# Kernel optimization log

Hardware: AMD Instinct MI355X
Metric: run time of the kernel (lower is better)

Reference implementation:

```python
import jax, jax.numpy as jnp
import numpy as np

N_HEADS = 16  # must match init_kwargs
BIAS_SCALE = 0.1


def _src_grid(out_size, in_size):
    # torch F.interpolate bilinear, align_corners=False semantics
    scale = in_size / out_size
    src = jnp.clip((jnp.arange(out_size, dtype=jnp.float32) + 0.5) * scale - 0.5, 0.0)
    i0 = jnp.minimum(jnp.floor(src).astype(jnp.int32), in_size - 1)
    i1 = jnp.minimum(i0 + 1, in_size - 1)
    w = src - i0.astype(jnp.float32)
    return i0, i1, w


def _bilinear_resize(img, out_h, out_w):
    Hin, Win = img.shape[-2], img.shape[-1]
    r0, r1, wy = _src_grid(out_h, Hin)
    c0, c1, wx = _src_grid(out_w, Win)
    rows = img[:, r0, :] * (1.0 - wy)[None, :, None] + img[:, r1, :] * wy[None, :, None]
    return rows[:, :, c0] * (1.0 - wx)[None, None, :] + rows[:, :, c1] * wx[None, None, :]


def setup_inputs() -> dict:
    key = jax.random.key(0)
    ks = jax.random.split(key, 10)
    B, L, D, M, K = 4, 1024, 1024, 64, 32
    s = 0.02
    return {
        "x": jax.random.normal(ks[0], (B, L, D), dtype=jnp.float32),
        "harmonics": jax.random.normal(ks[1], (B, M, K), dtype=jnp.float32),
        "wq": jax.random.normal(ks[2], (D, D), dtype=jnp.float32) * s,
        "bq": jax.random.normal(ks[3], (D,), dtype=jnp.float32) * s,
        "wk": jax.random.normal(ks[4], (D, D), dtype=jnp.float32) * s,
        "bk": jax.random.normal(ks[5], (D,), dtype=jnp.float32) * s,
        "wv": jax.random.normal(ks[6], (D, D), dtype=jnp.float32) * s,
        "bv": jax.random.normal(ks[7], (D,), dtype=jnp.float32) * s,
        "wo": jax.random.normal(ks[8], (D, D), dtype=jnp.float32) * s,
        "bo": jax.random.normal(ks[9], (D,), dtype=jnp.float32) * s,
    }


def reference(x, harmonics, wq, bq, wk, bk, wv, bv, wo, bo):
    B, L, D = x.shape
    hd = D // N_HEADS
    scaling = hd ** -0.5

    def split_heads(t):  # [B, L, D] -> [B, H, L, hd]
        return t.reshape(B, L, N_HEADS, hd).transpose(0, 2, 1, 3)

    q = split_heads(x @ wq.T + bq)
    k = split_heads(x @ wk.T + bk)
    v = split_heads(x @ wv.T + bv)

    scores = jnp.einsum("bhqd,bhkd->bhqk", q, k) * scaling  # [B, H, L, L]

    gram = jnp.einsum("bmk,bnk->bmn", harmonics, harmonics)  # [B, M, M]
    bias = _bilinear_resize(gram, L, L)  # [B, L, L]
    scores = scores + BIAS_SCALE * bias[:, None, :, :]

    attn = jax.nn.softmax(scores, axis=-1)
    out = jnp.einsum("bhqk,bhkd->bhqd", attn, v)  # [B, H, L, hd]
    out = out.transpose(0, 2, 1, 3).reshape(B, L, D)
    return out @ wo.T + bo
```

## Files before the change

### kernel.cpp

```cpp
#include <hip/hip_runtime.h>


using short8  = __attribute__((ext_vector_type(8))) short;
using short4v = __attribute__((ext_vector_type(4))) short;
using float4v = __attribute__((ext_vector_type(4))) float;

#define MFMA16(a, b, c) __builtin_amdgcn_mfma_f32_16x16x32_bf16((a), (b), (c), 0, 0, 0)

#define LOG2E 1.44269504088896f

static __device__ __forceinline__ short f2bf(float f) {
    union { float f; unsigned u; } v; v.f = f;
    unsigned r = v.u + 0x7fffu + ((v.u >> 16) & 1u);
    return (short)(r >> 16);
}

static __device__ __forceinline__ unsigned pack2bf(float lo, float hi) {
    union { float f; unsigned u; } a, b;
    a.f = lo; b.f = hi;
    return __builtin_amdgcn_perm(b.u + 0x8000u, a.u + 0x8000u, 0x07060302u);
}

static __device__ __forceinline__ void dma16(const short* g, short* l) {
    __builtin_amdgcn_global_load_lds((const __attribute__((address_space(1))) void*)g,
                                     (__attribute__((address_space(3))) void*)l, 16, 0, 0);
}

__global__ __launch_bounds__(256) void convert_all(
    const float* __restrict__ x,  const float* __restrict__ wq,
    const float* __restrict__ wk, const float* __restrict__ wv,
    const float* __restrict__ wo, short* __restrict__ xb, short* __restrict__ wb) {
    int idx = blockIdx.x * 256 + threadIdx.x;
    for (int i = idx; i < 2097152; i += gridDim.x * 256) {
        const float* src; short* dst;
        if (i < 1048576) {
            src = x + (size_t)i * 4;
            dst = xb + (size_t)i * 4;
        } else {
            int j = i - 1048576;
            int sel = j >> 18;
            const float* w = (sel == 0) ? wq : (sel == 1) ? wk : (sel == 2) ? wv : wo;
            src = w + (size_t)(j & 262143) * 4;
            dst = wb + (size_t)j * 4;
        }
        float4v v = *(const float4v*)src;
        short4v o;
        o.x = f2bf(v.x); o.y = f2bf(v.y); o.z = f2bf(v.z); o.w = f2bf(v.w);
        *(short4v*)dst = o;
    }
}

__global__ __launch_bounds__(256) void fill_aug(const float* __restrict__ harm,
                                                short* __restrict__ Qp,
                                                short* __restrict__ Kp) {
    int b  = blockIdx.y;
    int lc = blockIdx.x;
    int tid = threadIdx.x;
    int ll = tid >> 3;
    int d8 = (tid & 7) * 8;
    int l  = lc * 32 + ll;

    __shared__ float hs[64][33];
    for (int i = tid; i < 2048; i += 256) hs[i >> 5][i & 31] = harm[(size_t)b * 2048 + i];
    __syncthreads();

    float src = (l + 0.5f) * 0.0625f - 0.5f;
    if (src < 0.f) src = 0.f;
    int r0 = (int)floorf(src); if (r0 > 63) r0 = 63;
    int r1 = r0 + 1;           if (r1 > 63) r1 = 63;
    float wy = src - (float)r0;

    float hr[32];
    #pragma unroll
    for (int k = 0; k < 32; k++) hr[k] = (1.f - wy) * hs[r0][k] + wy * hs[r1][k];

    short8 qa, ka;
    #pragma unroll
    for (int j = 0; j < 8; j++) {
        float g = 0.f;
        #pragma unroll
        for (int k = 0; k < 32; k++) g += hr[k] * hs[d8 + j][k];
        qa[j] = f2bf(0.1f * LOG2E * g);
    }
    #pragma unroll
    for (int j = 0; j < 8; j++) {
        float vv = 0.f;
        if (d8 + j == r0) vv += 1.f - wy;
        if (d8 + j == r1) vv += wy;
        ka[j] = f2bf(vv);
    }
    for (int h = 0; h < 16; h++) {
        size_t base = (((size_t)(b * 16 + h) * 1024 + l) << 7) + 64 + d8;
        *(short8*)(Qp + base) = qa;
        *(short8*)(Kp + base) = ka;
    }
}

template <int MODE>
__global__ __launch_bounds__(256, 2) void gemm_kernel(
    const short* __restrict__ A,
    const short* __restrict__ Wb,
    const float* __restrict__ B0, const float* __restrict__ B1, const float* __restrict__ B2,
    short* __restrict__ Qp, short* __restrict__ Kp, short* __restrict__ Vp,
    float* __restrict__ outF) {
    const int z = blockIdx.z;
    const short* W  = Wb + (size_t)z * 1048576;
    const float* Bs = (z == 0) ? B0 : ((z == 1) ? B1 : B2);

    __shared__ short Sm[2][8192];

    const int tid  = threadIdx.x;
    const int lane = tid & 63;
    const int wv   = tid >> 6;
    const int wm   = (wv >> 1) * 64;
    const int wn   = (wv & 1) * 64;
    const int l16  = lane & 15;
    const int quad = lane >> 4;
    const int bm   = blockIdx.x * 128;
    const int bn   = blockIdx.y * 128;

    const short* aSrc[2];
    const short* wSrc[2];
    #pragma unroll
    for (int j = 0; j < 2; j++) {
        int c = j * 256 + tid;
        int r = c >> 2, gs = (c & 3) ^ ((r >> 1) & 3);
        aSrc[j] = A + (size_t)(bm + r) * 1024 + gs * 8;
        wSrc[j] = W + (size_t)(bn + r) * 1024 + gs * 8;
    }
    const int fr = (quad ^ ((l16 >> 1) & 3)) * 8;
    int ai[4], bi[4];
    #pragma unroll
    for (int t = 0; t < 4; t++) {
        ai[t] = (wm + t * 16 + l16) * 32 + fr;
        bi[t] = 4096 + (wn + t * 16 + l16) * 32 + fr;
    }

    float4v zero4 = {0.f, 0.f, 0.f, 0.f};
    float4v acc[4][4];
    #pragma unroll
    for (int i = 0; i < 4; i++)
        #pragma unroll
        for (int j = 0; j < 4; j++) acc[i][j] = zero4;

    dma16(aSrc[0], &Sm[0][wv * 512]);
    dma16(aSrc[1], &Sm[0][2048 + wv * 512]);
    dma16(wSrc[0], &Sm[0][4096 + wv * 512]);
    dma16(wSrc[1], &Sm[0][6144 + wv * 512]);
    #pragma unroll
    for (int j = 0; j < 2; j++) { aSrc[j] += 32; wSrc[j] += 32; }
    __syncthreads();

    for (int kt = 0; kt < 32; kt++) {
        const int cur = kt & 1, nxt = cur ^ 1;
        if (kt < 31) {
            dma16(aSrc[0], &Sm[nxt][wv * 512]);
            dma16(aSrc[1], &Sm[nxt][2048 + wv * 512]);
            dma16(wSrc[0], &Sm[nxt][4096 + wv * 512]);
            dma16(wSrc[1], &Sm[nxt][6144 + wv * 512]);
            #pragma unroll
            for (int j = 0; j < 2; j++) { aSrc[j] += 32; wSrc[j] += 32; }
        }

        short8 af[4], bfr[4];
        #pragma unroll
        for (int mt = 0; mt < 4; mt++) af[mt]  = *(const short8*)&Sm[cur][ai[mt]];
        #pragma unroll
        for (int nt = 0; nt < 4; nt++) bfr[nt] = *(const short8*)&Sm[cur][bi[nt]];
        #pragma unroll
        for (int mt = 0; mt < 4; mt++)
            #pragma unroll
            for (int nt = 0; nt < 4; nt++)
                acc[mt][nt] = MFMA16(af[mt], bfr[nt], acc[mt][nt]);

        __syncthreads();
    }

    #pragma unroll
    for (int mt = 0; mt < 4; mt++)
        #pragma unroll
        for (int nt = 0; nt < 4; nt++) {
            int col = bn + wn + nt * 16 + l16;
            float bias = Bs[col];
            #pragma unroll
            for (int r = 0; r < 4; r++) {
                int row = bm + wm + mt * 16 + quad * 4 + r;
                float val = acc[mt][nt][r] + bias;
                if (MODE == 1) {
                    outF[(size_t)row * 1024 + col] = val;
                } else {
                    int b = row >> 10, l = row & 1023;
                    int h = col >> 6,  d = col & 63;
                    size_t bhl = (size_t)(b * 16 + h) * 1024 + l;
                    if (z == 0)      Qp[(bhl << 7) + d] = f2bf(val * (0.125f * LOG2E));
                    else if (z == 1) Kp[(bhl << 7) + d] = f2bf(val);
                    else {
                        int slot = (l & ~31) | (((l >> 2) & 3) << 3) |
                                   (((l >> 4) & 1) << 2) | (l & 3);
                        Vp[(((size_t)(b * 16 + h) * 64 + d) << 10) + slot] = f2bf(val);
                    }
                }
            }
        }
}

__global__ __launch_bounds__(256, 2)
void flash_kernel(const short* __restrict__ Qp,
                  const short* __restrict__ Kp,
                  const short* __restrict__ Vp,
                  short* __restrict__ AO) {
    const int h  = blockIdx.x;
    const int qb = blockIdx.y;
    const int b  = blockIdx.z;
    const int tid  = threadIdx.x;
    const int lane = tid & 63;
    const int w    = tid >> 6;
    const int l16  = lane & 15;
    const int quad = lane >> 4;
    const size_t bh = (size_t)(b * 16 + h);

    __shared__ short Ks[24576];
    __shared__ short Vs[12288];

    short8 qf[2][4];
    #pragma unroll
    for (int u = 0; u < 2; u++) {
        const short* Qb = Qp + ((bh * 1024 + qb * 128 + w * 32 + u * 16 + l16) << 7) + quad * 8;
        #pragma unroll
        for (int c = 0; c < 4; c++) qf[u][c] = *(const short8*)(Qb + c * 32);
    }

    const short* kSrc[4];
    #pragma unroll
    for (int jj = 0; jj < 4; jj++) {
        int key = w * 16 + jj * 4 + quad;
        kSrc[jj] = Kp + (bh << 17) + key * 128 + ((l16 ^ (key & 15)) * 8);
    }
    const short* vSrc[2];
    #pragma unroll
    for (int g = 0; g < 2; g++) {
        int d = w * 16 + g * 8 + (lane >> 3);
        vSrc[g] = Vp + (bh << 16) + d * 1024 + (((lane & 7) ^ (d & 7)) * 8);
    }

    int krd[4];
    #pragma unroll
    for (int c = 0; c < 4; c++) krd[c] = l16 * 128 + (((c * 4 + quad) ^ l16) * 8);
    int vrd[2];
    #pragma unroll
    for (int g = 0; g < 2; g++) vrd[g] = l16 * 64 + (((g * 4 + quad) ^ (l16 & 7)) * 8);

    #pragma unroll
    for (int jj = 0; jj < 4; jj++) dma16(kSrc[jj], &Ks[w * 2048 + jj * 512]);
    #pragma unroll
    for (int g = 0; g < 2; g++) dma16(vSrc[g], &Vs[w * 1024 + g * 512]);
    #pragma unroll
    for (int jj = 0; jj < 4; jj++) kSrc[jj] += 8192;
    #pragma unroll
    for (int g = 0; g < 2; g++) vSrc[g] += 64;
    #pragma unroll
    for (int jj = 0; jj < 4; jj++) dma16(kSrc[jj], &Ks[8192 + w * 2048 + jj * 512]);
    #pragma unroll
    for (int g = 0; g < 2; g++) dma16(vSrc[g], &Vs[4096 + w * 1024 + g * 512]);
    #pragma unroll
    for (int jj = 0; jj < 4; jj++) kSrc[jj] += 8192;
    #pragma unroll
    for (int g = 0; g < 2; g++) vSrc[g] += 64;

    float4v zero4 = {0.f, 0.f, 0.f, 0.f};
    float4v o_acc[2][4];
    #pragma unroll
    for (int u = 0; u < 2; u++)
        #pragma unroll
        for (int mt = 0; mt < 4; mt++) o_acc[u][mt] = zero4;
    float4v l_acc[2] = {zero4, zero4};

    asm volatile("s_waitcnt vmcnt(6)" ::: "memory");
    __builtin_amdgcn_s_barrier();
    __builtin_amdgcn_sched_barrier(0);

    int bufR = 0;
    int bufW = 2;

    for (int kt = 0; kt < 16; kt++) {
        if (kt < 14) {
            const int wb = bufW << 13;
            const int wv2 = bufW << 12;
            #pragma unroll
            for (int jj = 0; jj < 4; jj++) dma16(kSrc[jj], &Ks[wb + w * 2048 + jj * 512]);
            #pragma unroll
            for (int g = 0; g < 2; g++) dma16(vSrc[g], &Vs[wv2 + w * 1024 + g * 512]);
            #pragma unroll
            for (int jj = 0; jj < 4; jj++) kSrc[jj] += 8192;
            #pragma unroll
            for (int g = 0; g < 2; g++) vSrc[g] += 64;
        }
        const int kb = bufR << 13;
        const int vb = bufR << 12;

        float4v s[2][4];
        #pragma unroll
        for (int mt = 0; mt < 4; mt++) {
            short8 kf[4];
            #pragma unroll
            for (int c = 0; c < 4; c++) kf[c] = *(const short8*)&Ks[kb + krd[c] + mt * 2048];
            #pragma unroll
            for (int u = 0; u < 2; u++) {
                s[u][mt] = MFMA16(kf[0], qf[u][0], zero4);
                #pragma unroll
                for (int c = 1; c < 4; c++)
                    s[u][mt] = MFMA16(kf[c], qf[u][c], s[u][mt]);
            }
        }

        #pragma unroll
        for (int u = 0; u < 2; u++)
            #pragma unroll
            for (int mt = 0; mt < 4; mt++) {
                #pragma unroll
                for (int r = 0; r < 4; r++)
                    s[u][mt][r] = __builtin_exp2f(s[u][mt][r]);
                #pragma unroll
                for (int r = 0; r < 4; r++)
                    l_acc[u][r] += s[u][mt][r];
            }

        #pragma unroll
        for (int g = 0; g < 2; g++) {
            short8 pf[2];
            #pragma unroll
            for (int u = 0; u < 2; u++) {
                union { unsigned uu[4]; short8 v; } t;
                t.uu[0] = pack2bf(s[u][2 * g][0], s[u][2 * g][1]);
                t.uu[1] = pack2bf(s[u][2 * g][2], s[u][2 * g][3]);
                t.uu[2] = pack2bf(s[u][2 * g + 1][0], s[u][2 * g + 1][1]);
                t.uu[3] = pack2bf(s[u][2 * g + 1][2], s[u][2 * g + 1][3]);
                pf[u] = t.v;
            }
            #pragma unroll
            for (int mt = 0; mt < 4; mt++) {
                short8 vf = *(const short8*)&Vs[vb + vrd[g] + mt * 1024];
                #pragma unroll
                for (int u = 0; u < 2; u++)
                    o_acc[u][mt] = MFMA16(vf, pf[u], o_acc[u][mt]);
            }
        }

        if (kt < 15) {
            if (kt < 14) {
                asm volatile("s_waitcnt vmcnt(6)" ::: "memory");
            } else {
                asm volatile("s_waitcnt vmcnt(0)" ::: "memory");
            }
            __builtin_amdgcn_s_barrier();
            __builtin_amdgcn_sched_barrier(0);
        }
        bufR = (bufR >= 2) ? 0 : bufR + 1;
        bufW = (bufW >= 2) ? 0 : bufW + 1;
    }

    #pragma unroll
    for (int u = 0; u < 2; u++) {
        float l = l_acc[u][0] + l_acc[u][1] + l_acc[u][2] + l_acc[u][3];
        l += __shfl_xor(l, 16, 64);
        l += __shfl_xor(l, 32, 64);
        float inv = 1.0f / l;
        int row = b * 1024 + qb * 128 + w * 32 + u * 16 + l16;
        #pragma unroll
        for (int mt = 0; mt < 4; mt++) {
            short4v ov;
            #pragma unroll
            for (int r = 0; r < 4; r++) ov[r] = f2bf(o_acc[u][mt][r] * inv);
            *(short4v*)(AO + (size_t)row * 1024 + h * 64 + mt * 16 + quad * 4) = ov;
        }
    }
}

extern "C" void kernel_launch(void* const* d_in, const int* in_sizes, int n_in,
                              void* d_out, int out_size, void* d_ws, size_t ws_size,
                              hipStream_t stream) {
    const float* x    = (const float*)d_in[0];
    const float* harm = (const float*)d_in[1];
    const float* wq   = (const float*)d_in[2];
    const float* bq   = (const float*)d_in[3];
    const float* wk   = (const float*)d_in[4];
    const float* bk   = (const float*)d_in[5];
    const float* wv   = (const float*)d_in[6];
    const float* bv   = (const float*)d_in[7];
    const float* wo   = (const float*)d_in[8];
    const float* bo   = (const float*)d_in[9];
    float* outF = (float*)d_out;

    short* xb   = (short*)d_ws;
    short* Qp   = xb + (size_t)4 * 1048576;
    short* Kp   = Qp + (size_t)8 * 1048576;
    short* Vp   = Kp + (size_t)8 * 1048576;
    short* Wqkv = Vp + (size_t)4 * 1048576;
    short* Wob  = Wqkv + (size_t)3 * 1048576;
    short* AO   = xb;

    convert_all<<<dim3(2048), dim3(256), 0, stream>>>(x, wq, wk, wv, wo, xb, Wqkv);
    gemm_kernel<0><<<dim3(32, 8, 3), dim3(256), 0, stream>>>(
        xb, Wqkv, bq, bk, bv, Qp, Kp, Vp, nullptr);
    fill_aug<<<dim3(32, 4), dim3(256), 0, stream>>>(harm, Qp, Kp);
    flash_kernel<<<dim3(16, 8, 4), dim3(256), 0, stream>>>(Qp, Kp, Vp, AO);
    gemm_kernel<1><<<dim3(32, 8, 1), dim3(256), 0, stream>>>(
        AO, Wob, bo, nullptr, nullptr, nullptr, nullptr, nullptr, outF);
}
```

Baseline: 193.2 us.

## Triple-buffer GEMM LDS tiles with partial vmcnt waits

Converts the projection GEMM's double-buffered LDS staging into a three-stage ring. Two tiles are prefetched up front, and each iteration waits only until the older DMA group has landed (vmcnt(4)) rather than fully synchronizing. This keeps two global-to-LDS loads in flight to hide memory latency. LDS use rises from 32KB to 48KB per block and launch bounds are raised to 3 blocks per CU, which tightens the register budget and may force spills.

```diff
diff --git a/kernel.cpp b/kernel.cpp
--- a/kernel.cpp
+++ b/kernel.cpp
@@ -97,7 +97,7 @@
 }
 
 template <int MODE>
-__global__ __launch_bounds__(256, 2) void gemm_kernel(
+__global__ __launch_bounds__(256, 3) void gemm_kernel(
     const short* __restrict__ A,
     const short* __restrict__ Wb,
     const float* __restrict__ B0, const float* __restrict__ B1, const float* __restrict__ B2,
@@ -107,7 +107,7 @@
     const short* W  = Wb + (size_t)z * 1048576;
     const float* Bs = (z == 0) ? B0 : ((z == 1) ? B1 : B2);
 
-    __shared__ short Sm[2][8192];
+    __shared__ short Sm[3][8192];
 
     const int tid  = threadIdx.x;
     const int lane = tid & 63;
@@ -149,31 +149,54 @@
     dma16(wSrc[1], &Sm[0][6144 + wv * 512]);
     #pragma unroll
     for (int j = 0; j < 2; j++) { aSrc[j] += 32; wSrc[j] += 32; }
-    __syncthreads();
+    dma16(aSrc[0], &Sm[1][wv * 512]);
+    dma16(aSrc[1], &Sm[1][2048 + wv * 512]);
+    dma16(wSrc[0], &Sm[1][4096 + wv * 512]);
+    dma16(wSrc[1], &Sm[1][6144 + wv * 512]);
+    #pragma unroll
+    for (int j = 0; j < 2; j++) { aSrc[j] += 32; wSrc[j] += 32; }
+
+    asm volatile("s_waitcnt vmcnt(4)" ::: "memory");
+    __builtin_amdgcn_s_barrier();
+    __builtin_amdgcn_sched_barrier(0);
+
+    int bufR = 0;
+    int bufW = 2;
 
     for (int kt = 0; kt < 32; kt++) {
-        const int cur = kt & 1, nxt = cur ^ 1;
-        if (kt < 31) {
-            dma16(aSrc[0], &Sm[nxt][wv * 512]);
-            dma16(aSrc[1], &Sm[nxt][2048 + wv * 512]);
-            dma16(wSrc[0], &Sm[nxt][4096 + wv * 512]);
-            dma16(wSrc[1], &Sm[nxt][6144 + wv * 512]);
+        if (kt < 30) {
+            short* wbuf = &Sm[bufW][0];
+            dma16(aSrc[0], wbuf + wv * 512);
+            dma16(aSrc[1], wbuf + 2048 + wv * 512);
+            dma16(wSrc[0], wbuf + 4096 + wv * 512);
+            dma16(wSrc[1], wbuf + 6144 + wv * 512);
             #pragma unroll
             for (int j = 0; j < 2; j++) { aSrc[j] += 32; wSrc[j] += 32; }
         }
 
+        const short* rbuf = &Sm[bufR][0];
         short8 af[4], bfr[4];
         #pragma unroll
-        for (int mt = 0; mt < 4; mt++) af[mt]  = *(const short8*)&Sm[cur][ai[mt]];
-        #pragma unroll
-        for (int nt = 0; nt < 4; nt++) bfr[nt] = *(const short8*)&Sm[cur][bi[nt]];
+        for (int mt = 0; mt < 4; mt++) af[mt]  = *(const short8*)&rbuf[ai[mt]];
+        #pragma unroll
+        for (int nt = 0; nt < 4; nt++) bfr[nt] = *(const short8*)&rbuf[bi[nt]];
         #pragma unroll
         for (int mt = 0; mt < 4; mt++)
             #pragma unroll
             for (int nt = 0; nt < 4; nt++)
                 acc[mt][nt] = MFMA16(af[mt], bfr[nt], acc[mt][nt]);
 
-        __syncthreads();
+        if (kt < 31) {
+            if (kt < 30) {
+                asm volatile("s_waitcnt vmcnt(4)" ::: "memory");
+            } else {
+                asm volatile("s_waitcnt vmcnt(0)" ::: "memory");
+            }
+            __builtin_amdgcn_s_barrier();
+            __builtin_amdgcn_sched_barrier(0);
+        }
+        bufR = (bufR >= 2) ? 0 : bufR + 1;
+        bufW = (bufW >= 2) ? 0 : bufW + 1;
     }
 
     #pragma unroll
```

New measurement: 192.9 us. Within noise of the previous version (-0.2%).
